# Kernel tuning notes

Hardware: AMD Instinct MI355X
Metric: run time of the kernel (lower is better)

The kernel has to match this reference:

```python
import jax, jax.numpy as jnp
import numpy as np

MASK_SUB = 1000000.0  # the module subtracts 1e6 from masked scores (not -inf)

def setup_inputs() -> dict:
    key = jax.random.key(0)
    kq, kk, kv = jax.random.split(key, 3)
    B, S, D = 16, 2048, 64
    q = jax.random.normal(kq, (B, S, D), dtype=jnp.float32)
    k = jax.random.normal(kk, (B, S, D), dtype=jnp.float32)
    v = jax.random.normal(kv, (B, S, D), dtype=jnp.float32)
    return {"q": q, "k": k, "v": v}

def reference(q, k, v):
    d_k = k.shape[-1]
    s = k.shape[-2]
    # scores: [b, s_q, s_k]
    scores = jnp.einsum('bqd,bkd->bqk', q, k) / jnp.sqrt(jnp.asarray(d_k, q.dtype))
    # causal mask: strictly-upper-triangular entries get 1e6 subtracted (matches torch.triu diagonal=1)
    causal = jnp.triu(jnp.ones((s, s), dtype=bool), k=1)
    scores = jnp.where(causal[None, :, :], scores - MASK_SUB, scores)
    weights = jax.nn.softmax(scores, axis=-1)
    return jnp.einsum('bqk,bkd->bqd', weights, v)
```

## Files before the change

### kernel.cpp

```cpp
#include <hip/hip_runtime.h>
#include <stdint.h>


typedef __bf16 bf16x8 __attribute__((ext_vector_type(8)));
typedef float f32x4 __attribute__((ext_vector_type(4)));

#define NB 16
#define SL 2048
#define DH 64

__device__ __forceinline__ __bf16 f2bf(float f) {
    uint32_t u = __builtin_bit_cast(uint32_t, f);
    u += 0x7FFFu + ((u >> 16) & 1u);
    uint16_t h = (uint16_t)(u >> 16);
    return __builtin_bit_cast(__bf16, h);
}

__device__ __forceinline__ void load_lds16(const void* g, void* l) {
    __builtin_amdgcn_global_load_lds(
        (const __attribute__((address_space(1))) uint32_t*)g,
        (__attribute__((address_space(3))) uint32_t*)l, 16, 0, 0);
}

__global__ __launch_bounds__(256) void prepass(
        const float* __restrict__ K, const float* __restrict__ V,
        __bf16* __restrict__ Kb, __bf16* __restrict__ Vt) {
    __shared__ float tl[64][68];
    const int b    = blockIdx.x >> 5;
    const int tile = blockIdx.x & 31;
    const int s0   = tile << 6;
    const int t    = threadIdx.x;
    const int r    = t >> 2;
    const int c0   = (t & 3) * 16;

    const float* Kp = K + ((size_t)(b * SL + s0) + r) * DH + c0;
    float4 f0 = ((const float4*)Kp)[0], f1 = ((const float4*)Kp)[1];
    float4 f2 = ((const float4*)Kp)[2], f3 = ((const float4*)Kp)[3];
    bf16x8 w0, w1;
    w0[0]=f2bf(f0.x); w0[1]=f2bf(f0.y); w0[2]=f2bf(f0.z); w0[3]=f2bf(f0.w);
    w0[4]=f2bf(f1.x); w0[5]=f2bf(f1.y); w0[6]=f2bf(f1.z); w0[7]=f2bf(f1.w);
    w1[0]=f2bf(f2.x); w1[1]=f2bf(f2.y); w1[2]=f2bf(f2.z); w1[3]=f2bf(f2.w);
    w1[4]=f2bf(f3.x); w1[5]=f2bf(f3.y); w1[6]=f2bf(f3.z); w1[7]=f2bf(f3.w);
    __bf16* Kbp = Kb + ((size_t)(b * SL + s0) + r) * DH;
    const int j0 = c0 >> 3;
    *(bf16x8*)(Kbp + ((j0       ^ (r & 7)) * 8)) = w0;
    *(bf16x8*)(Kbp + (((j0 + 1) ^ (r & 7)) * 8)) = w1;

    const float* Vp = V + ((size_t)(b * SL + s0) + r) * DH + c0;
    ((float4*)&tl[r][c0])[0] = ((const float4*)Vp)[0];
    ((float4*)&tl[r][c0])[1] = ((const float4*)Vp)[1];
    ((float4*)&tl[r][c0])[2] = ((const float4*)Vp)[2];
    ((float4*)&tl[r][c0])[3] = ((const float4*)Vp)[3];
    __syncthreads();

    __bf16* img = Vt + ((size_t)(b * 32 + tile)) * 4096;
#pragma unroll
    for (int half = 0; half < 2; ++half) {
        const int c = half * 256 + t;
        const int d = c >> 3, slot = c & 7;
        const int jj = slot ^ (d & 7);
        bf16x8 w;
#pragma unroll
        for (int e = 0; e < 8; ++e) w[e] = f2bf(tl[jj * 8 + e][d]);
        *(bf16x8*)(img + c * 8) = w;
    }
}

__global__ __launch_bounds__(256, 4) void attn_fwd(
        const float* __restrict__ Q, const __bf16* __restrict__ Kb,
        const __bf16* __restrict__ Vt, float* __restrict__ part,
        float* __restrict__ lpart) {
    __shared__ __align__(16) __bf16 lK[2][4096];
    __shared__ __align__(16) __bf16 lV[2][4096];
    __shared__ __align__(16) __bf16 lP[4][1024];

    const int bid = blockIdx.x;
    const int b   = bid & 15;
    const int j   = 79 - (bid >> 4);
    int T, c;
    if (j < 8)        { T = j;                 c = 0; }
    else if (j < 24)  { T = 8 + ((j - 8) >> 1);  c = (j - 8) & 1; }
    else if (j < 48)  { int k = j - 24; T = 16 + k / 3; c = k % 3; }
    else              { int k = j - 48; T = 24 + (k >> 2); c = k & 3; }
    const int kt0 = c * 8;
    const int kt1 = min(kt0 + 8, T + 1);

    const int tid  = threadIdx.x;
    const int wave = tid >> 6, lane = tid & 63, quad = lane >> 4, l16 = lane & 15;
    const int xk   = l16 & 7;
    const int qglob = T * 64 + wave * 16 + l16;

    const float QSC = 0.125f * 1.44269504088896340736f;
    bf16x8 qf[2];
    const float* qp = Q + ((size_t)b * SL + qglob) * DH;
#pragma unroll
    for (int s = 0; s < 2; ++s) {
        float4 a0 = ((const float4*)(qp + s * 32 + quad * 8))[0];
        float4 a1 = ((const float4*)(qp + s * 32 + quad * 8))[1];
        qf[s][0] = f2bf(a0.x * QSC); qf[s][1] = f2bf(a0.y * QSC);
        qf[s][2] = f2bf(a0.z * QSC); qf[s][3] = f2bf(a0.w * QSC);
        qf[s][4] = f2bf(a1.x * QSC); qf[s][5] = f2bf(a1.y * QSC);
        qf[s][6] = f2bf(a1.z * QSC); qf[s][7] = f2bf(a1.w * QSC);
    }

    bf16x8 ones;
#pragma unroll
    for (int e = 0; e < 8; ++e) ones[e] = __builtin_bit_cast(__bf16, (uint16_t)0x3F80);

    f32x4 acc[4];
#pragma unroll
    for (int t = 0; t < 4; ++t) acc[t] = (f32x4)0.0f;
    f32x4 accl = (f32x4)0.0f;

    const __bf16* Kbase = Kb + (size_t)b * SL * DH;
    const __bf16* Vbase = Vt + (size_t)b * 32 * 4096;
    __bf16* lPw = lP[wave];

    auto stage = [&](int kt2) {
        const int bufi = kt2 & 1;
        const __bf16* Ks = Kbase + (size_t)kt2 * 4096;
        const __bf16* Vs = Vbase + (size_t)kt2 * 4096;
#pragma unroll
        for (int i2 = 0; i2 < 2; ++i2) {
            load_lds16(Ks + (size_t)(i2 * 256 + tid) * 8,
                       &lK[bufi][(i2 * 256 + wave * 64) * 8]);
            load_lds16(Vs + (size_t)(i2 * 256 + tid) * 8,
                       &lV[bufi][(i2 * 256 + wave * 64) * 8]);
        }
    };

    stage(kt0);
    for (int kt = kt0; kt < kt1; ++kt) {
        __syncthreads();
        if (kt + 1 < kt1) stage(kt + 1);
        const __bf16* K_ = lK[kt & 1];
        const __bf16* V_ = lV[kt & 1];

        f32x4 sc[4];
#pragma unroll
        for (int t = 0; t < 4; ++t) sc[t] = (f32x4)0.0f;
        __builtin_amdgcn_s_setprio(1);
#pragma unroll
        for (int s = 0; s < 2; ++s) {
#pragma unroll
            for (int t = 0; t < 4; ++t) {
                bf16x8 kf = *(const bf16x8*)&K_[(t * 16 + l16) * 64 + (((s * 4 + quad) ^ xk) << 3)];
                sc[t] = __builtin_amdgcn_mfma_f32_16x16x32_bf16(kf, qf[s], sc[t], 0, 0, 0);
            }
        }
        __builtin_amdgcn_s_setprio(0);

        if (kt == T) {
            const int kb = kt * 64;
#pragma unroll
            for (int t = 0; t < 4; ++t)
#pragma unroll
                for (int r = 0; r < 4; ++r)
                    if (kb + t * 16 + quad * 4 + r > qglob) sc[t][r] = -1.0e30f;
        }

#pragma unroll
        for (int t = 0; t < 4; ++t) {
            float p0 = __builtin_amdgcn_exp2f(sc[t][0]);
            float p1 = __builtin_amdgcn_exp2f(sc[t][1]);
            float p2 = __builtin_amdgcn_exp2f(sc[t][2]);
            float p3 = __builtin_amdgcn_exp2f(sc[t][3]);
            uint32_t u0 = __builtin_amdgcn_perm(__builtin_bit_cast(uint32_t, p1),
                                               __builtin_bit_cast(uint32_t, p0), 0x07060302u);
            uint32_t u1 = __builtin_amdgcn_perm(__builtin_bit_cast(uint32_t, p3),
                                               __builtin_bit_cast(uint32_t, p2), 0x07060302u);
            const int cw = 2 * t + (quad >> 1);
            uint2 val; val.x = u0; val.y = u1;
            *(uint2*)&lPw[l16 * 64 + ((cw ^ xk) << 3) + ((quad & 1) << 2)] = val;
        }
        asm volatile("" ::: "memory");

        bf16x8 pf0 = *(const bf16x8*)&lPw[l16 * 64 + (((0 + quad) ^ xk) << 3)];
        bf16x8 pf1 = *(const bf16x8*)&lPw[l16 * 64 + (((4 + quad) ^ xk) << 3)];
        __builtin_amdgcn_s_setprio(1);
        accl = __builtin_amdgcn_mfma_f32_16x16x32_bf16(ones, pf0, accl, 0, 0, 0);
        accl = __builtin_amdgcn_mfma_f32_16x16x32_bf16(ones, pf1, accl, 0, 0, 0);

#pragma unroll
        for (int t = 0; t < 4; ++t) {
            bf16x8 vf = *(const bf16x8*)&V_[(t * 16 + l16) * 64 + (((0 + quad) ^ xk) << 3)];
            acc[t] = __builtin_amdgcn_mfma_f32_16x16x32_bf16(vf, pf0, acc[t], 0, 0, 0);
        }
#pragma unroll
        for (int t = 0; t < 4; ++t) {
            bf16x8 vf = *(const bf16x8*)&V_[(t * 16 + l16) * 64 + (((4 + quad) ^ xk) << 3)];
            acc[t] = __builtin_amdgcn_mfma_f32_16x16x32_bf16(vf, pf1, acc[t], 0, 0, 0);
        }
        __builtin_amdgcn_s_setprio(0);
    }

    float* pp = part + ((size_t)(b * SL + qglob) * 4 + c) * DH + quad * 4;
#pragma unroll
    for (int t = 0; t < 4; ++t) {
        float4 o4;
        o4.x = acc[t][0]; o4.y = acc[t][1]; o4.z = acc[t][2]; o4.w = acc[t][3];
        *(float4*)(pp + t * 16) = o4;
    }
    if (quad == 0)
        lpart[(size_t)(b * SL + qglob) * 4 + c] = accl[0];
}

__global__ __launch_bounds__(256) void combine(
        const float* __restrict__ part, const float* __restrict__ lpart,
        float* __restrict__ O) {
    const int tid = threadIdx.x;
    const int r   = blockIdx.x * 16 + (tid >> 4);
    const int d4  = tid & 15;
    const int T   = (r >> 6) & 31;
    const int nch = (T >> 3) + 1;
    float4 s = make_float4(0.f, 0.f, 0.f, 0.f);
    float ls = 0.f;
    for (int c = 0; c < nch; ++c) {
        float4 p = *(const float4*)(part + ((size_t)r * 4 + c) * DH + d4 * 4);
        s.x += p.x; s.y += p.y; s.z += p.z; s.w += p.w;
        ls += lpart[(size_t)r * 4 + c];
    }
    const float inv = 1.0f / ls;
    float4 o; o.x = s.x * inv; o.y = s.y * inv; o.z = s.z * inv; o.w = s.w * inv;
    *(float4*)(O + (size_t)r * DH + d4 * 4) = o;
}

extern "C" void kernel_launch(void* const* d_in, const int* in_sizes, int n_in,
                              void* d_out, int out_size, void* d_ws, size_t ws_size,
                              hipStream_t stream) {
    const float* q = (const float*)d_in[0];
    const float* k = (const float*)d_in[1];
    const float* v = (const float*)d_in[2];
    float* o = (float*)d_out;
    __bf16* Kb   = (__bf16*)d_ws;
    __bf16* Vt   = Kb + (size_t)NB * SL * DH;
    float*  pt   = (float*)((char*)d_ws + (8u << 20));
    float*  lp   = pt + (size_t)NB * SL * 4 * DH;
    hipLaunchKernelGGL(prepass, dim3(NB * 32), dim3(256), 0, stream, k, v, Kb, Vt);
    hipLaunchKernelGGL(attn_fwd, dim3(1280), dim3(256), 0, stream, q, Kb, Vt, pt, lp);
    hipLaunchKernelGGL(combine, dim3(NB * SL / 16), dim3(256), 0, stream, pt, lp, o);
}
```

Measured before the change: 99.83 us.

## Process two 64-row query tiles per wave to reuse K/V LDS loads

Each block now handles 128 query rows: every wave computes two 16-row query strips that share the same K and V fragments read from LDS, so K/V staging and LDS reads are amortised over twice the compute. The grid is halved and the chunk-to-block mapping and the combine's chunk count are recomputed for 128-row tiles. The row-sum is now accumulated with scalar adds and cross-lane shuffles rather than extra MFMAs against a ones vector. This raises register pressure (occupancy bound lowered to 3 waves per SIMD) and doubles the LDS P buffer, and there are fewer blocks to balance the causal workload.

```diff
diff --git a/kernel.cpp b/kernel.cpp
--- a/kernel.cpp
+++ b/kernel.cpp
@@ -66,51 +66,52 @@
     }
 }
 
-__global__ __launch_bounds__(256, 4) void attn_fwd(
+__global__ __launch_bounds__(256, 3) void attn_fwd(
         const float* __restrict__ Q, const __bf16* __restrict__ Kb,
         const __bf16* __restrict__ Vt, float* __restrict__ part,
         float* __restrict__ lpart) {
     __shared__ __align__(16) __bf16 lK[2][4096];
     __shared__ __align__(16) __bf16 lV[2][4096];
-    __shared__ __align__(16) __bf16 lP[4][1024];
+    __shared__ __align__(16) __bf16 lP[4][2048];
 
     const int bid = blockIdx.x;
     const int b   = bid & 15;
-    const int j   = 79 - (bid >> 4);
-    int T, c;
-    if (j < 8)        { T = j;                 c = 0; }
-    else if (j < 24)  { T = 8 + ((j - 8) >> 1);  c = (j - 8) & 1; }
-    else if (j < 48)  { int k = j - 24; T = 16 + k / 3; c = k % 3; }
-    else              { int k = j - 48; T = 24 + (k >> 2); c = k & 3; }
+    const int j   = 39 - (bid >> 4);
+    int qb, c;
+    if (j < 4)        { qb = j;                 c = 0; }
+    else if (j < 12)  { qb = 4 + ((j - 4) >> 1);  c = (j - 4) & 1; }
+    else if (j < 24)  { int k = j - 12; qb = 8 + k / 3;    c = k % 3; }
+    else              { int k = j - 24; qb = 12 + (k >> 2); c = k & 3; }
+    const int nt  = 2 * qb + 2;
     const int kt0 = c * 8;
-    const int kt1 = min(kt0 + 8, T + 1);
+    const int kt1 = min(kt0 + 8, nt);
 
     const int tid  = threadIdx.x;
     const int wave = tid >> 6, lane = tid & 63, quad = lane >> 4, l16 = lane & 15;
     const int xk   = l16 & 7;
-    const int qglob = T * 64 + wave * 16 + l16;
+    const int qg0  = qb * 128 + wave * 16 + l16;
+    const int qg1  = qg0 + 64;
 
     const float QSC = 0.125f * 1.44269504088896340736f;
-    bf16x8 qf[2];
-    const float* qp = Q + ((size_t)b * SL + qglob) * DH;
-#pragma unroll
-    for (int s = 0; s < 2; ++s) {
-        float4 a0 = ((const float4*)(qp + s * 32 + quad * 8))[0];
-        float4 a1 = ((const float4*)(qp + s * 32 + quad * 8))[1];
-        qf[s][0] = f2bf(a0.x * QSC); qf[s][1] = f2bf(a0.y * QSC);
-        qf[s][2] = f2bf(a0.z * QSC); qf[s][3] = f2bf(a0.w * QSC);
-        qf[s][4] = f2bf(a1.x * QSC); qf[s][5] = f2bf(a1.y * QSC);
-        qf[s][6] = f2bf(a1.z * QSC); qf[s][7] = f2bf(a1.w * QSC);
-    }
-
-    bf16x8 ones;
-#pragma unroll
-    for (int e = 0; e < 8; ++e) ones[e] = __builtin_bit_cast(__bf16, (uint16_t)0x3F80);
-
-    f32x4 acc[4];
-#pragma unroll
-    for (int t = 0; t < 4; ++t) acc[t] = (f32x4)0.0f;
-    f32x4 accl = (f32x4)0.0f;
+    bf16x8 qf[2][2];
+#pragma unroll
+    for (int st = 0; st < 2; ++st) {
+        const float* qp = Q + ((size_t)b * SL + (st ? qg1 : qg0)) * DH;
+#pragma unroll
+        for (int s = 0; s < 2; ++s) {
+            float4 a0 = ((const float4*)(qp + s * 32 + quad * 8))[0];
+            float4 a1 = ((const float4*)(qp + s * 32 + quad * 8))[1];
+            qf[st][s][0] = f2bf(a0.x * QSC); qf[st][s][1] = f2bf(a0.y * QSC);
+            qf[st][s][2] = f2bf(a0.z * QSC); qf[st][s][3] = f2bf(a0.w * QSC);
+            qf[st][s][4] = f2bf(a1.x * QSC); qf[st][s][5] = f2bf(a1.y * QSC);
+            qf[st][s][6] = f2bf(a1.z * QSC); qf[st][s][7] = f2bf(a1.w * QSC);
+        }
+    }
+
+    f32x4 acc0[4], acc1[4];
+#pragma unroll
+    for (int t = 0; t < 4; ++t) { acc0[t] = (f32x4)0.0f; acc1[t] = (f32x4)0.0f; }
+    float ls0 = 0.0f, ls1 = 0.0f;
 
     const __bf16* Kbase = Kb + (size_t)b * SL * DH;
     const __bf16* Vbase = Vt + (size_t)b * 32 * 4096;
@@ -126,6 +127,24 @@
                        &lK[bufi][(i2 * 256 + wave * 64) * 8]);
             load_lds16(Vs + (size_t)(i2 * 256 + tid) * 8,
                        &lV[bufi][(i2 * 256 + wave * 64) * 8]);
+        }
+    };
+
+    auto softmax_store = [&](f32x4* sc, int soff, float& ls) {
+#pragma unroll
+        for (int t = 0; t < 4; ++t) {
+            float p0 = __builtin_amdgcn_exp2f(sc[t][0]);
+            float p1 = __builtin_amdgcn_exp2f(sc[t][1]);
+            float p2 = __builtin_amdgcn_exp2f(sc[t][2]);
+            float p3 = __builtin_amdgcn_exp2f(sc[t][3]);
+            ls += (p0 + p1) + (p2 + p3);
+            uint32_t u0 = __builtin_amdgcn_perm(__builtin_bit_cast(uint32_t, p1),
+                                               __builtin_bit_cast(uint32_t, p0), 0x07060302u);
+            uint32_t u1 = __builtin_amdgcn_perm(__builtin_bit_cast(uint32_t, p3),
+                                               __builtin_bit_cast(uint32_t, p2), 0x07060302u);
+            const int cw = 2 * t + (quad >> 1);
+            uint2 val; val.x = u0; val.y = u1;
+            *(uint2*)&lPw[soff + l16 * 64 + ((cw ^ xk) << 3) + ((quad & 1) << 2)] = val;
         }
     };
 
@@ -136,73 +155,75 @@
         const __bf16* K_ = lK[kt & 1];
         const __bf16* V_ = lV[kt & 1];
 
-        f32x4 sc[4];
-#pragma unroll
-        for (int t = 0; t < 4; ++t) sc[t] = (f32x4)0.0f;
+        f32x4 sc0[4], sc1[4];
+#pragma unroll
+        for (int t = 0; t < 4; ++t) { sc0[t] = (f32x4)0.0f; sc1[t] = (f32x4)0.0f; }
         __builtin_amdgcn_s_setprio(1);
 #pragma unroll
         for (int s = 0; s < 2; ++s) {
 #pragma unroll
             for (int t = 0; t < 4; ++t) {
                 bf16x8 kf = *(const bf16x8*)&K_[(t * 16 + l16) * 64 + (((s * 4 + quad) ^ xk) << 3)];
-                sc[t] = __builtin_amdgcn_mfma_f32_16x16x32_bf16(kf, qf[s], sc[t], 0, 0, 0);
+                sc0[t] = __builtin_amdgcn_mfma_f32_16x16x32_bf16(kf, qf[0][s], sc0[t], 0, 0, 0);
+                sc1[t] = __builtin_amdgcn_mfma_f32_16x16x32_bf16(kf, qf[1][s], sc1[t], 0, 0, 0);
             }
         }
         __builtin_amdgcn_s_setprio(0);
 
-        if (kt == T) {
+        if (kt >= 2 * qb) {
             const int kb = kt * 64;
 #pragma unroll
             for (int t = 0; t < 4; ++t)
 #pragma unroll
-                for (int r = 0; r < 4; ++r)
-                    if (kb + t * 16 + quad * 4 + r > qglob) sc[t][r] = -1.0e30f;
-        }
-
-#pragma unroll
-        for (int t = 0; t < 4; ++t) {
-            float p0 = __builtin_amdgcn_exp2f(sc[t][0]);
-            float p1 = __builtin_amdgcn_exp2f(sc[t][1]);
-            float p2 = __builtin_amdgcn_exp2f(sc[t][2]);
-            float p3 = __builtin_amdgcn_exp2f(sc[t][3]);
-            uint32_t u0 = __builtin_amdgcn_perm(__builtin_bit_cast(uint32_t, p1),
-                                               __builtin_bit_cast(uint32_t, p0), 0x07060302u);
-            uint32_t u1 = __builtin_amdgcn_perm(__builtin_bit_cast(uint32_t, p3),
-                                               __builtin_bit_cast(uint32_t, p2), 0x07060302u);
-            const int cw = 2 * t + (quad >> 1);
-            uint2 val; val.x = u0; val.y = u1;
-            *(uint2*)&lPw[l16 * 64 + ((cw ^ xk) << 3) + ((quad & 1) << 2)] = val;
-        }
+                for (int r = 0; r < 4; ++r) {
+                    const int key = kb + t * 16 + quad * 4 + r;
+                    if (key > qg0) sc0[t][r] = -1.0e30f;
+                    if (key > qg1) sc1[t][r] = -1.0e30f;
+                }
+        }
+
+        softmax_store(sc0, 0,    ls0);
+        softmax_store(sc1, 1024, ls1);
         asm volatile("" ::: "memory");
 
-        bf16x8 pf0 = *(const bf16x8*)&lPw[l16 * 64 + (((0 + quad) ^ xk) << 3)];
-        bf16x8 pf1 = *(const bf16x8*)&lPw[l16 * 64 + (((4 + quad) ^ xk) << 3)];
+        bf16x8 pf00 = *(const bf16x8*)&lPw[       l16 * 64 + (((0 + quad) ^ xk) << 3)];
+        bf16x8 pf01 = *(const bf16x8*)&lPw[       l16 * 64 + (((4 + quad) ^ xk) << 3)];
+        bf16x8 pf10 = *(const bf16x8*)&lPw[1024 + l16 * 64 + (((0 + quad) ^ xk) << 3)];
+        bf16x8 pf11 = *(const bf16x8*)&lPw[1024 + l16 * 64 + (((4 + quad) ^ xk) << 3)];
+
         __builtin_amdgcn_s_setprio(1);
-        accl = __builtin_amdgcn_mfma_f32_16x16x32_bf16(ones, pf0, accl, 0, 0, 0);
-        accl = __builtin_amdgcn_mfma_f32_16x16x32_bf16(ones, pf1, accl, 0, 0, 0);
-
 #pragma unroll
         for (int t = 0; t < 4; ++t) {
             bf16x8 vf = *(const bf16x8*)&V_[(t * 16 + l16) * 64 + (((0 + quad) ^ xk) << 3)];
-            acc[t] = __builtin_amdgcn_mfma_f32_16x16x32_bf16(vf, pf0, acc[t], 0, 0, 0);
+            acc0[t] = __builtin_amdgcn_mfma_f32_16x16x32_bf16(vf, pf00, acc0[t], 0, 0, 0);
+            acc1[t] = __builtin_amdgcn_mfma_f32_16x16x32_bf16(vf, pf10, acc1[t], 0, 0, 0);
         }
 #pragma unroll
         for (int t = 0; t < 4; ++t) {
             bf16x8 vf = *(const bf16x8*)&V_[(t * 16 + l16) * 64 + (((4 + quad) ^ xk) << 3)];
-            acc[t] = __builtin_amdgcn_mfma_f32_16x16x32_bf16(vf, pf1, acc[t], 0, 0, 0);
+            acc0[t] = __builtin_amdgcn_mfma_f32_16x16x32_bf16(vf, pf01, acc0[t], 0, 0, 0);
+            acc1[t] = __builtin_amdgcn_mfma_f32_16x16x32_bf16(vf, pf11, acc1[t], 0, 0, 0);
         }
         __builtin_amdgcn_s_setprio(0);
     }
 
-    float* pp = part + ((size_t)(b * SL + qglob) * 4 + c) * DH + quad * 4;
+    ls0 += __shfl_xor(ls0, 16); ls0 += __shfl_xor(ls0, 32);
+    ls1 += __shfl_xor(ls1, 16); ls1 += __shfl_xor(ls1, 32);
+
+    float* pp0 = part + ((size_t)(b * SL + qg0) * 4 + c) * DH + quad * 4;
+    float* pp1 = part + ((size_t)(b * SL + qg1) * 4 + c) * DH + quad * 4;
 #pragma unroll
     for (int t = 0; t < 4; ++t) {
         float4 o4;
-        o4.x = acc[t][0]; o4.y = acc[t][1]; o4.z = acc[t][2]; o4.w = acc[t][3];
-        *(float4*)(pp + t * 16) = o4;
-    }
-    if (quad == 0)
-        lpart[(size_t)(b * SL + qglob) * 4 + c] = accl[0];
+        o4.x = acc0[t][0]; o4.y = acc0[t][1]; o4.z = acc0[t][2]; o4.w = acc0[t][3];
+        *(float4*)(pp0 + t * 16) = o4;
+        o4.x = acc1[t][0]; o4.y = acc1[t][1]; o4.z = acc1[t][2]; o4.w = acc1[t][3];
+        *(float4*)(pp1 + t * 16) = o4;
+    }
+    if (quad == 0) {
+        lpart[(size_t)(b * SL + qg0) * 4 + c] = ls0;
+        lpart[(size_t)(b * SL + qg1) * 4 + c] = ls1;
+    }
 }
 
 __global__ __launch_bounds__(256) void combine(
@@ -211,8 +232,8 @@
     const int tid = threadIdx.x;
     const int r   = blockIdx.x * 16 + (tid >> 4);
     const int d4  = tid & 15;
-    const int T   = (r >> 6) & 31;
-    const int nch = (T >> 3) + 1;
+    const int qb  = (r >> 7) & 15;
+    const int nch = (2 * qb + 9) >> 3;
     float4 s = make_float4(0.f, 0.f, 0.f, 0.f);
     float ls = 0.f;
     for (int c = 0; c < nch; ++c) {
@@ -237,6 +258,6 @@
     float*  pt   = (float*)((char*)d_ws + (8u << 20));
     float*  lp   = pt + (size_t)NB * SL * 4 * DH;
     hipLaunchKernelGGL(prepass, dim3(NB * 32), dim3(256), 0, stream, k, v, Kb, Vt);
-    hipLaunchKernelGGL(attn_fwd, dim3(1280), dim3(256), 0, stream, q, Kb, Vt, pt, lp);
+    hipLaunchKernelGGL(attn_fwd, dim3(640), dim3(256), 0, stream, q, Kb, Vt, pt, lp);
     hipLaunchKernelGGL(combine, dim3(NB * SL / 16), dim3(256), 0, stream, pt, lp, o);
 }
```

After: 100.2 us. No clear change (+0.4%).
